# Performance work log

Hardware: AMD Instinct MI355X
Metric: run time of the kernel (lower is better)

The kernel has to match this reference:

```python
import jax, jax.numpy as jnp
import numpy as np

B, S, D, H = 2, 2048, 2048, 16
DH = D // H  # 128 head dim
ROPE_THETA = 10000.0
LN_EPS = 1e-5


def setup_inputs() -> dict:
    key = jax.random.key(0)
    k1, k2, k3 = jax.random.split(key, 3)
    positions = jnp.broadcast_to(jnp.arange(S, dtype=jnp.int64), (B, S))
    hidden_states = jax.random.normal(k1, (B, S, D), dtype=jnp.float32)
    w_qkv = jax.random.normal(k2, (D, 3 * D), dtype=jnp.float32) * 0.02
    w_out = jax.random.normal(k3, (D, D), dtype=jnp.float32) * 0.02
    return {"positions": positions, "hidden_states": hidden_states,
            "w_qkv": w_qkv, "w_out": w_out}


def _rope(x, positions):
    # NeoX-style rotary (vLLM get_rope default): rotate split halves.
    # x: [B, S, H, DH], positions: [B, S]
    half = DH // 2
    inv_freq = 1.0 / (ROPE_THETA ** (jnp.arange(0, half, dtype=jnp.float32) / half))
    ang = positions.astype(jnp.float32)[..., None] * inv_freq  # [B, S, half]
    cos = jnp.cos(ang)[:, :, None, :]  # [B, S, 1, half]
    sin = jnp.sin(ang)[:, :, None, :]
    x1, x2 = x[..., :half], x[..., half:]
    return jnp.concatenate([x1 * cos - x2 * sin, x2 * cos + x1 * sin], axis=-1)


def reference(positions, hidden_states, w_qkv, w_out):
    # LayerNorm with no affine params (elementwise_affine=False)
    mu = jnp.mean(hidden_states, axis=-1, keepdims=True)
    var = jnp.mean(jnp.square(hidden_states - mu), axis=-1, keepdims=True)
    x = (hidden_states - mu) * jax.lax.rsqrt(var + LN_EPS)

    qkv = jnp.einsum('bsd,de->bse', x, w_qkv)  # [B, S, 3D]
    q, k, v = jnp.split(qkv, 3, axis=-1)
    q = q.reshape(B, S, H, DH)
    k = k.reshape(B, S, H, DH)
    v = v.reshape(B, S, H, DH)

    q = _rope(q, positions)
    k = _rope(k, positions)

    scale = DH ** -0.5
    scores = jnp.einsum('bqhd,bkhd->bhqk', q, k) * scale  # [B, H, S, S]
    causal = jnp.tril(jnp.ones((S, S), dtype=bool))
    scores = jnp.where(causal, scores, jnp.finfo(scores.dtype).min)
    probs = jax.nn.softmax(scores, axis=-1)
    attn = jnp.einsum('bhqk,bkhd->bqhd', probs, v).reshape(B, S, D)

    return jnp.einsum('bsd,de->bse', attn, w_out)
```

## Files before the change

kernel.cpp:

```cpp
#include <hip/hip_runtime.h>


typedef __bf16 bf16x8 __attribute__((ext_vector_type(8)));
typedef float f32x4 __attribute__((ext_vector_type(4)));

__device__ __forceinline__ unsigned short f2bf(float f) {
  unsigned u = __builtin_bit_cast(unsigned, f);
  u = u + 0x7fffu + ((u >> 16) & 1u);
  return (unsigned short)(u >> 16);
}
__device__ __forceinline__ float bf2f(unsigned short h) {
  unsigned u = ((unsigned)h) << 16;
  return __builtin_bit_cast(float, u);
}

#define GLD_LDS16(gp, lp)                                                      \
  __builtin_amdgcn_global_load_lds((__attribute__((address_space(1))) void*)(gp), \
                                   (__attribute__((address_space(3))) void*)(lp), \
                                   16, 0, 0)

__global__ __launch_bounds__(256) void prep_kernel(const float* __restrict__ hs,
                                                   const float* __restrict__ wqkv,
                                                   const float* __restrict__ wout,
                                                   unsigned short* __restrict__ xb,
                                                   unsigned short* __restrict__ wqkvT,
                                                   unsigned short* __restrict__ woutT) {
  const int tid = threadIdx.x;
  int bx = blockIdx.x;
  if (bx < 4096) {
    const float* rp = hs + (size_t)bx * 2048;
    const float4 v0 = ((const float4*)rp)[tid];
    const float4 v1 = ((const float4*)rp)[tid + 256];
    float s  = v0.x + v0.y + v0.z + v0.w + v1.x + v1.y + v1.z + v1.w;
    float ss = v0.x*v0.x + v0.y*v0.y + v0.z*v0.z + v0.w*v0.w
             + v1.x*v1.x + v1.y*v1.y + v1.z*v1.z + v1.w*v1.w;
#pragma unroll
    for (int m = 1; m < 64; m <<= 1) { s += __shfl_xor(s, m); ss += __shfl_xor(ss, m); }
    __shared__ float rs[4], rss[4];
    if ((tid & 63) == 0) { rs[tid >> 6] = s; rss[tid >> 6] = ss; }
    __syncthreads();
    s  = rs[0] + rs[1] + rs[2] + rs[3];
    ss = rss[0] + rss[1] + rss[2] + rss[3];
    const float mean = s * (1.0f / 2048.0f);
    const float var  = ss * (1.0f / 2048.0f) - mean * mean;
    const float inv  = rsqrtf(var + 1e-5f);
    ushort4 o0, o1;
    o0.x = f2bf((v0.x - mean) * inv); o0.y = f2bf((v0.y - mean) * inv);
    o0.z = f2bf((v0.z - mean) * inv); o0.w = f2bf((v0.w - mean) * inv);
    o1.x = f2bf((v1.x - mean) * inv); o1.y = f2bf((v1.y - mean) * inv);
    o1.z = f2bf((v1.z - mean) * inv); o1.w = f2bf((v1.w - mean) * inv);
    ushort4* op = (ushort4*)(xb + (size_t)bx * 2048);
    op[tid] = o0; op[tid + 256] = o1;
    return;
  }
  bx -= 4096;
  const int bxx = bx & 255, byy = bx >> 8;
  const float* in;
  unsigned short* out;
  int N, n0;
  if (bxx < 192) { in = wqkv; out = wqkvT; N = 6144; n0 = bxx * 32; }
  else           { in = wout; out = woutT; N = 2048; n0 = (bxx - 192) * 32; }
  const int k0 = byy * 32;
  const int tx = tid & 31, ty = tid >> 5;
  __shared__ float t[32][33];
#pragma unroll
  for (int i = 0; i < 4; i++)
    t[ty + i * 8][tx] = in[(size_t)(k0 + ty + i * 8) * N + n0 + tx];
  __syncthreads();
#pragma unroll
  for (int i = 0; i < 4; i++)
    out[(size_t)(n0 + ty + i * 8) * 2048 + k0 + tx] = f2bf(t[tx][ty + i * 8]);
}

template <int OUT_BF16>
__global__ __launch_bounds__(256) void gemm_bt(const unsigned short* __restrict__ A,
                                               const unsigned short* __restrict__ Bt,
                                               void* __restrict__ Cv,
                                               int M, int N, int K) {
  __shared__ alignas(16) unsigned short sA[128 * 64];
  __shared__ alignas(16) unsigned short sB[128 * 64];
  const int tid = threadIdx.x;
  const int lane = tid & 63, wave = tid >> 6;
  const int wm = wave >> 1, wn = wave & 1;
  const int ln15 = lane & 15, quad = lane >> 4;
  const size_t m0 = (size_t)blockIdx.y * 128, n0 = (size_t)blockIdx.x * 128;
  const unsigned short* Ag = A + m0 * (size_t)K;
  const unsigned short* Bg = Bt + n0 * (size_t)K;
  const int lr8 = lane >> 3;
  const int sc8 = ((lane & 7) ^ (lr8 & 7)) * 8;
  const int xk = ln15 & 7;

  f32x4 acc[4][4];
#pragma unroll
  for (int mi = 0; mi < 4; mi++)
#pragma unroll
    for (int ni = 0; ni < 4; ni++) acc[mi][ni] = (f32x4){0.f, 0.f, 0.f, 0.f};

  const int iters = K >> 6;
  for (int kt = 0; kt < iters; ++kt) {
    const int kb = kt * 64;
    __syncthreads();
#pragma unroll
    for (int i = 0; i < 4; i++) {
      const int c = wave * 4 + i;
      const int row = c * 8 + lr8;
      GLD_LDS16(Ag + (size_t)row * K + kb + sc8, &sA[c * 512]);
      GLD_LDS16(Bg + (size_t)row * K + kb + sc8, &sB[c * 512]);
    }
    __syncthreads();
#pragma unroll
    for (int ks = 0; ks < 2; ks++) {
      bf16x8 af[4], bf[4];
#pragma unroll
      for (int mi = 0; mi < 4; mi++)
        af[mi] = *(const bf16x8*)&sA[(wm * 64 + mi * 16 + ln15) * 64 +
                                     ((ks * 4 + quad) ^ xk) * 8];
#pragma unroll
      for (int ni = 0; ni < 4; ni++)
        bf[ni] = *(const bf16x8*)&sB[(wn * 64 + ni * 16 + ln15) * 64 +
                                     ((ks * 4 + quad) ^ xk) * 8];
#pragma unroll
      for (int mi = 0; mi < 4; mi++)
#pragma unroll
        for (int ni = 0; ni < 4; ni++)
          acc[mi][ni] = __builtin_amdgcn_mfma_f32_16x16x32_bf16(af[mi], bf[ni], acc[mi][ni], 0, 0, 0);
    }
  }
#pragma unroll
  for (int mi = 0; mi < 4; mi++)
#pragma unroll
    for (int ni = 0; ni < 4; ni++) {
      const size_t col = n0 + wn * 64 + ni * 16 + ln15;
#pragma unroll
      for (int r = 0; r < 4; r++) {
        const size_t row = m0 + wm * 64 + mi * 16 + quad * 4 + r;
        if (OUT_BF16)
          ((unsigned short*)Cv)[row * N + col] = f2bf(acc[mi][ni][r]);
        else
          ((float*)Cv)[row * N + col] = acc[mi][ni][r];
      }
    }
}

__global__ __launch_bounds__(256) void rv_kernel(const unsigned short* __restrict__ qkv,
                                                 unsigned short* __restrict__ Qo,
                                                 unsigned short* __restrict__ Ko,
                                                 unsigned short* __restrict__ VT) {
  const int tid = threadIdx.x;
  const int bx = blockIdx.x;
  if (bx < 2048) {
    const int t = bx * 256 + tid;
    const int g = t & 7;
    const int h = (t >> 3) & 15;
    const int row = t >> 7;
    const int s = row & 2047;
    const size_t base = (size_t)row * 6144 + h * 128 + g * 8;
    const bf16x8 q1 = *(const bf16x8*)&qkv[base];
    const bf16x8 q2 = *(const bf16x8*)&qkv[base + 64];
    const bf16x8 k1 = *(const bf16x8*)&qkv[base + 2048];
    const bf16x8 k2 = *(const bf16x8*)&qkv[base + 2048 + 64];
    const float qscale = 0.08838834764831845f;
    bf16x8 oq1, oq2, ok1, ok2;
#pragma unroll
    for (int j = 0; j < 8; j++) {
      const int i = g * 8 + j;
      const float freq = exp2f(-(float)i * (13.287712379549449f / 64.0f));
      float rev = (float)s * freq * 0.15915494309189535f;
      rev -= floorf(rev);
      const float ar = rev * 6.283185307179586f;
      const float sn = __sinf(ar), cs = __cosf(ar);
      const float a1 = (float)q1[j], a2 = (float)q2[j];
      const float b1 = (float)k1[j], b2 = (float)k2[j];
      oq1[j] = (__bf16)((a1 * cs - a2 * sn) * qscale);
      oq2[j] = (__bf16)((a2 * cs + a1 * sn) * qscale);
      ok1[j] = (__bf16)(b1 * cs - b2 * sn);
      ok2[j] = (__bf16)(b2 * cs + b1 * sn);
    }
    const size_t ob = ((size_t)(((row >> 11) << 4) + h) * 2048 + s) * 128 + g * 8;
    *(bf16x8*)&Qo[ob]      = oq1;
    *(bf16x8*)&Qo[ob + 64] = oq2;
    *(bf16x8*)&Ko[ob]      = ok1;
    *(bf16x8*)&Ko[ob + 64] = ok2;
    return;
  }
  const int idx = bx - 2048;
  const int s0 = (idx & 63) * 32;
  const int d0 = ((idx >> 6) & 3) * 32;
  const int bh = idx >> 8, b = bh >> 4, h = bh & 15;
  const int tx = tid & 31, ty = tid >> 5;
  __shared__ unsigned short t[32][34];
#pragma unroll
  for (int i = 0; i < 4; i++)
    t[ty + i * 8][tx] =
        qkv[(size_t)(b * 2048 + s0 + ty + i * 8) * 6144 + 4096 + h * 128 + d0 + tx];
  __syncthreads();
#pragma unroll
  for (int i = 0; i < 4; i++)
    VT[((size_t)bh * 128 + d0 + ty + i * 8) * 2048 + s0 + tx] = t[tx][ty + i * 8];
}

__global__ __launch_bounds__(256) void flash_kernel(const unsigned short* __restrict__ Q,
                                                    const unsigned short* __restrict__ Kbuf,
                                                    const unsigned short* __restrict__ VT,
                                                    unsigned short* __restrict__ attn) {
  __shared__ alignas(16) unsigned short sK[2][64 * 128];
  __shared__ alignas(16) unsigned short sVT[2][128 * 64];
  __shared__ alignas(16) unsigned short sP[64 * 72];

  const int bh = blockIdx.y;
  const int b = bh >> 4, h = bh & 15;
  const int tid = threadIdx.x;
  const int lane = tid & 63, w = tid >> 6;
  const int ln15 = lane & 15, quad = lane >> 4;

  const unsigned short* Qg = Q + (size_t)bh * 2048 * 128;
  const unsigned short* Kg = Kbuf + (size_t)bh * 2048 * 128;
  const unsigned short* Vg = VT + (size_t)bh * 128 * 2048;

  const float L2E = 1.44269504088896f;
  bf16x8 onesf;
#pragma unroll
  for (int j = 0; j < 8; j++) onesf[j] = (__bf16)1.0f;

  const int kcrow = (lane >> 4);
  const int kch = (lane & 15);
  const int vcrow = (lane >> 3);
  const int vch = (lane & 7);

#pragma unroll 1
  for (int t = 0; t < 2; t++) {
    const int qt = t ? (31 - (int)blockIdx.x) : (int)blockIdx.x;
    const int q0 = qt * 64;

    bf16x8 qf[4];
#pragma unroll
    for (int ks = 0; ks < 4; ks++)
      qf[ks] = *(const bf16x8*)&Qg[(size_t)(q0 + w * 16 + ln15) * 128 + ks * 32 + quad * 8];

    f32x4 o[8], ol;
#pragma unroll
    for (int nd = 0; nd < 8; nd++) o[nd] = (f32x4){0.f, 0.f, 0.f, 0.f};
    ol = (f32x4){0.f, 0.f, 0.f, 0.f};
    float mrow[4];
#pragma unroll
    for (int r = 0; r < 4; r++) mrow[r] = -1e30f;

    __syncthreads();
#pragma unroll
    for (int i = 0; i < 4; i++) {
      const int c = w * 4 + i;
      const int row = c * 4 + kcrow;
      GLD_LDS16(Kg + (size_t)row * 128 + (kch ^ (row & 15)) * 8, &sK[0][c * 512]);
    }
#pragma unroll
    for (int i = 0; i < 4; i++) {
      const int c = w * 4 + i;
      const int row = c * 8 + vcrow;
      GLD_LDS16(Vg + (size_t)row * 2048 + (vch ^ (row & 7)) * 8, &sVT[0][c * 512]);
    }

#pragma unroll 1
    for (int j = 0; j <= qt; j++) {
      const int cur = j & 1;
      __syncthreads();
      if (j < qt) {
        const int k0n = (j + 1) * 64;
        const int nxt = cur ^ 1;
#pragma unroll
        for (int i = 0; i < 4; i++) {
          const int c = w * 4 + i;
          const int row = c * 4 + kcrow;
          GLD_LDS16(Kg + (size_t)(k0n + row) * 128 + (kch ^ (row & 15)) * 8, &sK[nxt][c * 512]);
        }
#pragma unroll
        for (int i = 0; i < 4; i++) {
          const int c = w * 4 + i;
          const int row = c * 8 + vcrow;
          GLD_LDS16(Vg + (size_t)row * 2048 + k0n + (vch ^ (row & 7)) * 8, &sVT[nxt][c * 512]);
        }
      }

      f32x4 sc[4];
#pragma unroll
      for (int ni = 0; ni < 4; ni++) sc[ni] = (f32x4){0.f, 0.f, 0.f, 0.f};
#pragma unroll
      for (int ks = 0; ks < 4; ks++) {
        bf16x8 bk[4];
#pragma unroll
        for (int ni = 0; ni < 4; ni++) {
          const int row = ni * 16 + ln15;
          const int ch = (ks * 4 + quad) ^ (row & 15);
          bk[ni] = *(const bf16x8*)&sK[cur][row * 128 + ch * 8];
        }
#pragma unroll
        for (int ni = 0; ni < 4; ni++)
          sc[ni] = __builtin_amdgcn_mfma_f32_16x16x32_bf16(qf[ks], bk[ni], sc[ni], 0, 0, 0);
      }

      float mt[4] = {-1e30f, -1e30f, -1e30f, -1e30f};
      if (j == qt) {
        const int k0 = j * 64;
#pragma unroll
        for (int ni = 0; ni < 4; ni++) {
          const int key = k0 + ni * 16 + ln15;
#pragma unroll
          for (int r = 0; r < 4; r++) {
            const int qrow = q0 + w * 16 + quad * 4 + r;
            float v = sc[ni][r];
            if (key > qrow) v = -1e30f;
            sc[ni][r] = v;
            mt[r] = fmaxf(mt[r], v);
          }
        }
      } else {
#pragma unroll
        for (int ni = 0; ni < 4; ni++)
#pragma unroll
          for (int r = 0; r < 4; r++) mt[r] = fmaxf(mt[r], sc[ni][r]);
      }
#pragma unroll
      for (int r = 0; r < 4; r++) {
        float m = mt[r];
        m = fmaxf(m, __shfl_xor(m, 1));
        m = fmaxf(m, __shfl_xor(m, 2));
        m = fmaxf(m, __shfl_xor(m, 4));
        m = fmaxf(m, __shfl_xor(m, 8));
        const float mnew = fmaxf(mrow[r], m);
        const float alpha = exp2f((mrow[r] - mnew) * L2E);
        mrow[r] = mnew;
#pragma unroll
        for (int ni = 0; ni < 4; ni++)
          sc[ni][r] = exp2f((sc[ni][r] - mnew) * L2E);
        ol[r] *= alpha;
#pragma unroll
        for (int nd = 0; nd < 8; nd++) o[nd][r] *= alpha;
      }
#pragma unroll
      for (int ni = 0; ni < 4; ni++)
#pragma unroll
        for (int r = 0; r < 4; r++)
          sP[(w * 16 + quad * 4 + r) * 72 + ni * 16 + ln15] = f2bf(sc[ni][r]);

      bf16x8 pf[2];
#pragma unroll
      for (int kk = 0; kk < 2; kk++)
        pf[kk] = *(const bf16x8*)&sP[(w * 16 + ln15) * 72 + kk * 32 + quad * 8];
#pragma unroll
      for (int kk = 0; kk < 2; kk++) {
#pragma unroll
        for (int nd = 0; nd < 8; nd++) {
          const int row = nd * 16 + ln15;
          const int ch = (kk * 4 + quad) ^ (row & 7);
          const bf16x8 bv = *(const bf16x8*)&sVT[cur][row * 64 + ch * 8];
          o[nd] = __builtin_amdgcn_mfma_f32_16x16x32_bf16(pf[kk], bv, o[nd], 0, 0, 0);
        }
        ol = __builtin_amdgcn_mfma_f32_16x16x32_bf16(pf[kk], onesf, ol, 0, 0, 0);
      }
    }

#pragma unroll
    for (int r = 0; r < 4; r++) {
      const float inv = 1.0f / ol[r];
      const int qrow = q0 + w * 16 + quad * 4 + r;
#pragma unroll
      for (int nd = 0; nd < 8; nd++) {
        const int d = nd * 16 + ln15;
        attn[((size_t)(b * 2048 + qrow)) * 2048 + h * 128 + d] = f2bf(o[nd][r] * inv);
      }
    }
  }
}

extern "C" void kernel_launch(void* const* d_in, const int* in_sizes, int n_in,
                              void* d_out, int out_size, void* d_ws, size_t ws_size,
                              hipStream_t stream) {
  const float* hs   = (const float*)d_in[1];
  const float* wqkv = (const float*)d_in[2];
  const float* wout = (const float*)d_in[3];
  float* out = (float*)d_out;
  char* ws = (char*)d_ws;

  unsigned short* x_bf  = (unsigned short*)(ws);
  unsigned short* wqkvT = (unsigned short*)(ws + 16777216);
  unsigned short* woutT = (unsigned short*)(ws + 41943040);
  unsigned short* qkv   = (unsigned short*)(ws + 50331648);
  unsigned short* Qb    = (unsigned short*)(ws + 100663296);
  unsigned short* Kb    = (unsigned short*)(ws + 117440512);
  unsigned short* VT    = wqkvT;
  unsigned short* attn  = x_bf;

  prep_kernel<<<4096 + 16384, 256, 0, stream>>>(hs, wqkv, wout, x_bf, wqkvT, woutT);
  gemm_bt<1><<<dim3(48, 32), 256, 0, stream>>>(x_bf, wqkvT, (void*)qkv, 4096, 6144, 2048);
  rv_kernel<<<2048 + 8192, 256, 0, stream>>>(qkv, Qb, Kb, VT);
  flash_kernel<<<dim3(16, 32), 256, 0, stream>>>(Qb, Kb, VT, attn);
  gemm_bt<0><<<dim3(16, 32), 256, 0, stream>>>(attn, woutT, (void*)out, 4096, 2048, 2048);
}
```

Baseline: 416.2 us.

## Use 256x256-tile 8-wave pipelined GEMM for QKV projection

Adds a new bf16 GEMM kernel for the QKV projection with 256x256 output tiles and 512 threads. A and B tiles are double-buffered in LDS and fed by direct global-to-LDS loads, with XOR swizzling. Each k-step is split into four phases, so prefetches of the next A tile and the tile after next of B overlap MFMA work, and MFMA sections run under raised wave priority. The larger tile is meant to cut global and LDS traffic per FLOP. In exchange it launches only 384 blocks and uses about 128KB of LDS per block, which can leave poor wave balance across CUs.

Measured after the change: 412.4 us. About the same (-0.9%).

```diff
diff --git a/kernel.cpp b/kernel.cpp
--- a/kernel.cpp
+++ b/kernel.cpp
@@ -140,6 +140,125 @@
           ((float*)Cv)[row * N + col] = acc[mi][ni][r];
       }
     }
+}
+
+__global__ __launch_bounds__(512, 2) void gemm256_bt(const unsigned short* __restrict__ A,
+                                                     const unsigned short* __restrict__ Bt,
+                                                     unsigned short* __restrict__ C,
+                                                     int M, int N, int K) {
+  __shared__ alignas(16) unsigned short sA[2][256 * 64];
+  __shared__ alignas(16) unsigned short sB[2][256 * 64];
+  const int tid = threadIdx.x;
+  const int lane = tid & 63, w = tid >> 6;
+  const int wm = w >> 2, wn = w & 3;
+  const int ln15 = lane & 15, quad = lane >> 4;
+  const size_t m0 = (size_t)blockIdx.y * 256, n0 = (size_t)blockIdx.x * 256;
+  const unsigned short* Ag = A + m0 * (size_t)K;
+  const unsigned short* Bg = Bt + n0 * (size_t)K;
+  const int lr8 = lane >> 3;
+  const int sc8 = ((lane & 7) ^ (lr8 & 7)) * 8;
+  const int xk = ln15 & 7;
+
+#define G256_STAGE_A(buf, h, kt)                                               \
+  {                                                                            \
+    _Pragma("unroll") for (int i_ = 0; i_ < 2; i_++) {                         \
+      const int c_ = w * 2 + i_;                                               \
+      const int row_ = c_ * 8 + lr8;                                           \
+      GLD_LDS16(Ag + (size_t)((h) * 128 + row_) * K + (size_t)(kt) * 64 + sc8, \
+                &sA[buf][(h) * 8192 + c_ * 512]);                              \
+    }                                                                          \
+  }
+#define G256_STAGE_B(buf, h, kt)                                               \
+  {                                                                            \
+    _Pragma("unroll") for (int i_ = 0; i_ < 2; i_++) {                         \
+      const int c_ = w * 2 + i_;                                               \
+      const int row_ = c_ * 8 + lr8;                                           \
+      GLD_LDS16(Bg + (size_t)((h) * 128 + row_) * K + (size_t)(kt) * 64 + sc8, \
+                &sB[buf][(h) * 8192 + c_ * 512]);                              \
+    }                                                                          \
+  }
+
+  f32x4 acc[8][4];
+#pragma unroll
+  for (int a = 0; a < 8; a++)
+#pragma unroll
+    for (int ni = 0; ni < 4; ni++) acc[a][ni] = (f32x4){0.f, 0.f, 0.f, 0.f};
+
+  const int nt = K >> 6;
+
+  G256_STAGE_A(0, 0, 0); G256_STAGE_A(0, 1, 0);
+  G256_STAGE_B(0, 0, 0); G256_STAGE_B(0, 1, 0);
+  G256_STAGE_B(1, 0, 1); G256_STAGE_B(1, 1, 1);
+  asm volatile("s_waitcnt vmcnt(4)" ::: "memory");
+  __builtin_amdgcn_s_barrier();
+
+#define G256_PHASE(P, Q, STMT, TAILSTMT)                                       \
+  {                                                                            \
+    bf16x8 af_[2][2];                                                          \
+    _Pragma("unroll") for (int mi = 0; mi < 2; mi++) {                         \
+      const int row = wm * 128 + (Q) * 32 + mi * 16 + ln15;                    \
+      _Pragma("unroll") for (int ks = 0; ks < 2; ks++)                         \
+        af_[mi][ks] = *(const bf16x8*)&sA[P][row * 64 +                        \
+                                            (((ks * 4 + quad) ^ xk) * 8)];     \
+    }                                                                          \
+    STMT                                                                       \
+    __builtin_amdgcn_s_barrier();                                              \
+    asm volatile("s_waitcnt lgkmcnt(0)" ::: "memory");                         \
+    __builtin_amdgcn_s_setprio(1);                                             \
+    _Pragma("unroll") for (int ks = 0; ks < 2; ks++)                           \
+      _Pragma("unroll") for (int mi = 0; mi < 2; mi++)                         \
+        _Pragma("unroll") for (int ni = 0; ni < 4; ni++)                       \
+          acc[(Q) * 2 + mi][ni] = __builtin_amdgcn_mfma_f32_16x16x32_bf16(     \
+              af_[mi][ks], bf_[ni][ks], acc[(Q) * 2 + mi][ni], 0, 0, 0);       \
+    __builtin_amdgcn_s_setprio(0);                                             \
+    TAILSTMT                                                                   \
+    __builtin_amdgcn_s_barrier();                                              \
+  }
+
+#define G256_ITER(KT, P)                                                       \
+  {                                                                            \
+    const int kt_ = (KT);                                                      \
+    bf16x8 bf_[4][2];                                                          \
+           \
+    _Pragma("unroll") for (int ni = 0; ni < 4; ni++) {                         \
+      const int row = wn * 64 + ni * 16 + ln15;                                \
+      _Pragma("unroll") for (int ks = 0; ks < 2; ks++)                         \
+        bf_[ni][ks] = *(const bf16x8*)&sB[P][row * 64 +                        \
+                                            (((ks * 4 + quad) ^ xk) * 8)];     \
+    }                                                                          \
+    G256_PHASE(P, 0,                                                           \
+      { if (kt_ + 1 < nt) G256_STAGE_A(P ^ 1, 0, kt_ + 1); }, {})              \
+    G256_PHASE(P, 1,                                                           \
+      { if (kt_ + 1 < nt) G256_STAGE_A(P ^ 1, 1, kt_ + 1); }, {})              \
+    G256_PHASE(P, 2,                                                           \
+      { if (kt_ + 2 < nt) G256_STAGE_B(P, 0, kt_ + 2); }, {})                  \
+    G256_PHASE(P, 3,                                                           \
+      { if (kt_ + 2 < nt) G256_STAGE_B(P, 1, kt_ + 2); },                      \
+      { if (kt_ + 2 < nt) { asm volatile("s_waitcnt vmcnt(4)" ::: "memory"); } \
+        else             { asm volatile("s_waitcnt vmcnt(0)" ::: "memory"); } })\
+  }
+
+#pragma unroll 1
+  for (int kt2 = 0; kt2 < nt; kt2 += 2) {
+    G256_ITER(kt2, 0)
+    G256_ITER(kt2 + 1, 1)
+  }
+
+#pragma unroll
+  for (int a = 0; a < 8; a++)
+#pragma unroll
+    for (int ni = 0; ni < 4; ni++) {
+      const size_t col = n0 + wn * 64 + ni * 16 + ln15;
+#pragma unroll
+      for (int r = 0; r < 4; r++) {
+        const size_t row = m0 + wm * 128 + a * 16 + quad * 4 + r;
+        C[row * N + col] = f2bf(acc[a][ni][r]);
+      }
+    }
+#undef G256_STAGE_A
+#undef G256_STAGE_B
+#undef G256_PHASE
+#undef G256_ITER
 }
 
 __global__ __launch_bounds__(256) void rv_kernel(const unsigned short* __restrict__ qkv,
@@ -390,7 +509,7 @@
   unsigned short* attn  = x_bf;
 
   prep_kernel<<<4096 + 16384, 256, 0, stream>>>(hs, wqkv, wout, x_bf, wqkvT, woutT);
-  gemm_bt<1><<<dim3(48, 32), 256, 0, stream>>>(x_bf, wqkvT, (void*)qkv, 4096, 6144, 2048);
+  gemm256_bt<<<dim3(24, 16), 512, 0, stream>>>(x_bf, wqkvT, qkv, 4096, 6144, 2048);
   rv_kernel<<<2048 + 8192, 256, 0, stream>>>(qkv, Qb, Kb, VT);
   flash_kernel<<<dim3(16, 32), 256, 0, stream>>>(Qb, Kb, VT, attn);
   gemm_bt<0><<<dim3(16, 32), 256, 0, stream>>>(attn, woutT, (void*)out, 4096, 2048, 2048);
```
